# Kernel tuning notes

Hardware: AMD Instinct MI355X
Metric: run time of the kernel (lower is better)

Reference implementation:

```python
import jax, jax.numpy as jnp
import numpy as np

T = 8192
F = 128   # feature_size
H = 2048  # hidden_size
PRED_LEN = 12  # pred_length (fc_out head exists in module but is unused in forward)


def setup_inputs() -> dict:
    key = jax.random.key(0)
    ks = jax.random.split(key, 10)
    s_ih = 1.0 / np.sqrt(H)
    inp = {
        "x": jax.random.normal(ks[0], (T, F), dtype=jnp.float32),
        # PyTorch nn.LSTM params, gate order [i, f, g, o]
        "W_ih": jax.random.uniform(ks[1], (4 * H, F), jnp.float32, -s_ih, s_ih),
        "W_hh": jax.random.uniform(ks[2], (4 * H, H), jnp.float32, -s_ih, s_ih),
        "b_ih": jax.random.uniform(ks[3], (4 * H,), jnp.float32, -s_ih, s_ih),
        "b_hh": jax.random.uniform(ks[4], (4 * H,), jnp.float32, -s_ih, s_ih),
        # self.linear: Linear(H, H)
        "W_lin": jax.random.uniform(ks[5], (H, H), jnp.float32, -s_ih, s_ih),
        "b_lin": jax.random.uniform(ks[6], (H,), jnp.float32, -s_ih, s_ih),
        # self.one_out: Linear(H, 2)
        "W_out": jax.random.uniform(ks[7], (2, H), jnp.float32, -s_ih, s_ih),
        "b_out": jax.random.uniform(ks[8], (2,), jnp.float32, -s_ih, s_ih),
    }
    return inp


def _lstm_last_h(x, W_ih, W_hh, b_ih, b_hh):
    # x: [T, F]; returns final hidden state h: [H]
    # Precompute input projections for all timesteps: [T, 4H]
    x_proj = x @ W_ih.T + (b_ih + b_hh)

    def step(carry, xp):
        h, c = carry
        gates = xp + h @ W_hh.T  # [4H]
        i = jax.nn.sigmoid(gates[0 * H:1 * H])
        f = jax.nn.sigmoid(gates[1 * H:2 * H])
        g = jnp.tanh(gates[2 * H:3 * H])
        o = jax.nn.sigmoid(gates[3 * H:4 * H])
        c = f * c + i * g
        h = o * jnp.tanh(c)
        return (h, c), None

    h0 = jnp.zeros((H,), x.dtype)
    c0 = jnp.zeros((H,), x.dtype)
    (h, _), _ = jax.lax.scan(step, (h0, c0), x_proj)
    return h


def reference(x, W_ih, W_hh, b_ih, b_hh, W_lin, b_lin, W_out, b_out):
    h = _lstm_last_h(x, W_ih, W_hh, b_ih, b_hh)        # [H]
    y = h @ W_lin.T + b_lin                            # [H]
    y = y @ W_out.T + b_out                            # [2]
    return y.reshape(1, 1, 2)                          # matches torch (1,1,2)
```

## Files before the change

### kernel.cpp

```cpp
#include <hip/hip_runtime.h>


#define H      2048
#define TSTEPS 8192
#define FEAT   128
#define NBLK   256
#define NTHR   512
#define RESET_TH 0x10000000u

typedef float vf4 __attribute__((ext_vector_type(4)));
typedef float vf2 __attribute__((ext_vector_type(2)));

__device__ __forceinline__ float sigm(float xv) {
  return __builtin_amdgcn_rcpf(1.0f + __expf(-xv));
}
__device__ __forceinline__ float tanh_(float xv) {
  return 1.0f - 2.0f * __builtin_amdgcn_rcpf(__expf(2.0f * xv) + 1.0f);
}

union F2U { unsigned long long u; float2 f; };

#define DECLG(g) vf4 w##g##_0, w##g##_1, w##g##_2, w##g##_3, \
                     w##g##_4, w##g##_5, w##g##_6, w##g##_7; \
                 vf2 wih##g; float bias##g; float acc##g;

#define LOADG(g) { \
  const int row_ = (g) * H + j; \
  const float* wr_ = W_hh + (long)row_ * H; \
  w##g##_0 = *(const vf4*)(wr_ + 4*(ln      )); \
  w##g##_1 = *(const vf4*)(wr_ + 4*(ln +  64)); \
  w##g##_2 = *(const vf4*)(wr_ + 4*(ln + 128)); \
  w##g##_3 = *(const vf4*)(wr_ + 4*(ln + 192)); \
  w##g##_4 = *(const vf4*)(wr_ + 4*(ln + 256)); \
  w##g##_5 = *(const vf4*)(wr_ + 4*(ln + 320)); \
  w##g##_6 = *(const vf4*)(wr_ + 4*(ln + 384)); \
  w##g##_7 = *(const vf4*)(wr_ + 4*(ln + 448)); \
  wih##g  = *(const vf2*)(W_ih + (long)row_ * FEAT + 2*ln); \
  bias##g = b_ih[row_] + b_hh[row_]; }

#define PIN(g) asm volatile("" : \
  "+v"(w##g##_0), "+v"(w##g##_1), "+v"(w##g##_2), "+v"(w##g##_3), \
  "+v"(w##g##_4), "+v"(w##g##_5), "+v"(w##g##_6), "+v"(w##g##_7), \
  "+v"(wih##g), "+v"(bias##g));

#define STAGE_CHUNK(k, src, ldsrow) { \
  F2U lo_, hi_; \
  const float* p_ = (src) + 4*(ln + 64*(k)); \
  lo_.u = __hip_atomic_load((const unsigned long long*)p_, \
                            __ATOMIC_RELAXED, __HIP_MEMORY_SCOPE_AGENT); \
  hi_.u = __hip_atomic_load((const unsigned long long*)(p_ + 2), \
                            __ATOMIC_RELAXED, __HIP_MEMORY_SCOPE_AGENT); \
  vf4 t_; t_.x = lo_.f.x; t_.y = lo_.f.y; t_.z = hi_.f.x; t_.w = hi_.f.y; \
  *(vf4*)&(ldsrow)[4*(ln + 64*(k))] = t_; }

#define LDSREAD(k, ldsrow) \
  const vf4 hv##k = *(const vf4*)&(ldsrow)[4*(ln + 64*(k))];

#define FMA_G(g, c) \
  acc##g = __builtin_fmaf(w##g##_##c.x, h4_.x, acc##g); \
  acc##g = __builtin_fmaf(w##g##_##c.y, h4_.y, acc##g); \
  acc##g = __builtin_fmaf(w##g##_##c.z, h4_.z, acc##g); \
  acc##g = __builtin_fmaf(w##g##_##c.w, h4_.w, acc##g);

#define FMA_C(c) { const vf4 h4_ = hv##c; \
  FMA_G(0, c) FMA_G(1, c) FMA_G(2, c) FMA_G(3, c) }

#define REDUCE(g) { float a_ = acc##g; \
  a_ += __shfl_xor(a_, 1);  a_ += __shfl_xor(a_, 2);  a_ += __shfl_xor(a_, 4); \
  a_ += __shfl_xor(a_, 8);  a_ += __shfl_xor(a_, 16); a_ += __shfl_xor(a_, 32); \
  acc##g = a_ + bias##g; }

__global__ __launch_bounds__(NTHR, 2)
void lstm_persist(const float* __restrict__ x,
                  const float* __restrict__ W_ih,
                  const float* __restrict__ W_hh,
                  const float* __restrict__ b_ih,
                  const float* __restrict__ b_hh,
                  const float* __restrict__ W_lin,
                  const float* __restrict__ b_lin,
                  const float* __restrict__ W_out,
                  const float* __restrict__ b_out,
                  float* __restrict__ out,
                  float* __restrict__ ws)
{
  const int tid = threadIdx.x;
  const int b   = blockIdx.x;
  const int wv  = tid >> 6;
  const int ln  = tid & 63;

  float* hbuf0 = ws;
  float* hbuf1 = ws + H;
  float* ylin  = ws + 2 * H;
  unsigned* leaves = (unsigned*)(ws + 4 * H);
  unsigned* myleaf = leaves + (b & 7) * 64;

  __shared__ __align__(16) float h_lds[2][H];

  if (tid == 0 && b < 8) {
    if (__hip_atomic_load(leaves + b * 64, __ATOMIC_RELAXED,
                          __HIP_MEMORY_SCOPE_AGENT) >= RESET_TH)
      __hip_atomic_store(leaves + b * 64, 0u, __ATOMIC_RELAXED,
                         __HIP_MEMORY_SCOPE_AGENT);
  }
  if (tid < 8) {
    while (__hip_atomic_load(leaves + tid * 64, __ATOMIC_RELAXED,
                             __HIP_MEMORY_SCOPE_AGENT) >= RESET_TH) {
      __builtin_amdgcn_s_sleep(1);
    }
  }

  *(vf4*)&h_lds[0][4 * tid] = (vf4)(0.0f);

  const int j = b * 8 + wv;
  DECLG(0) DECLG(1) DECLG(2) DECLG(3)
  LOADG(0) LOADG(1) LOADG(2) LOADG(3)
  PIN(0) PIN(1) PIN(2) PIN(3)

  __syncthreads();

  float cst = 0.0f;

  #pragma unroll 1
  for (int t = 0; t < TSTEPS; ++t) {
    const vf2 xr = *(const vf2*)(x + (long)t * FEAT + 2 * ln);
    float* ldsrow = h_lds[t & 1];

    if (t > 0 && wv == 0) {
      const unsigned target = 32u * (unsigned)t;
      if (ln < 8) {
        const unsigned* lp = leaves + ln * 64;
        while (__hip_atomic_load(lp, __ATOMIC_RELAXED,
                                 __HIP_MEMORY_SCOPE_AGENT) < target) {
          __builtin_amdgcn_s_sleep(1);
        }
      }
      __builtin_amdgcn_fence(__ATOMIC_ACQUIRE, "workgroup");
      const float* hsrc = (t & 1) ? hbuf1 : hbuf0;
      STAGE_CHUNK(0, hsrc, ldsrow) STAGE_CHUNK(1, hsrc, ldsrow)
      STAGE_CHUNK(2, hsrc, ldsrow) STAGE_CHUNK(3, hsrc, ldsrow)
      STAGE_CHUNK(4, hsrc, ldsrow) STAGE_CHUNK(5, hsrc, ldsrow)
      STAGE_CHUNK(6, hsrc, ldsrow) STAGE_CHUNK(7, hsrc, ldsrow)
    }
    __syncthreads();

    LDSREAD(0, ldsrow) LDSREAD(1, ldsrow) LDSREAD(2, ldsrow) LDSREAD(3, ldsrow)
    LDSREAD(4, ldsrow) LDSREAD(5, ldsrow) LDSREAD(6, ldsrow) LDSREAD(7, ldsrow)

    acc0 = wih0.x * xr.x + wih0.y * xr.y;
    acc1 = wih1.x * xr.x + wih1.y * xr.y;
    acc2 = wih2.x * xr.x + wih2.y * xr.y;
    acc3 = wih3.x * xr.x + wih3.y * xr.y;

    FMA_C(0) FMA_C(1) FMA_C(2) FMA_C(3)
    FMA_C(4) FMA_C(5) FMA_C(6) FMA_C(7)

    REDUCE(0) REDUCE(1) REDUCE(2) REDUCE(3)

    const float iv = sigm(acc0);
    const float fv = sigm(acc1);
    const float gv = tanh_(acc2);
    const float ov = sigm(acc3);
    cst = fv * cst + iv * gv;
    const float hval = ov * tanh_(cst);

    if (ln == 0) {
      float* hdst = ((t + 1) & 1) ? hbuf1 : hbuf0;
      __hip_atomic_store(hdst + j, hval, __ATOMIC_RELAXED,
                         __HIP_MEMORY_SCOPE_AGENT);
    }
    __syncthreads();
    if (tid == 0) {
      __hip_atomic_fetch_add(myleaf, 1u, __ATOMIC_RELAXED,
                             __HIP_MEMORY_SCOPE_AGENT);
    }
  }

  {
    float* ldsrow = h_lds[0];
    if (wv == 0) {
      const unsigned target = 32u * (unsigned)TSTEPS;
      if (ln < 8) {
        const unsigned* lp = leaves + ln * 64;
        while (__hip_atomic_load(lp, __ATOMIC_RELAXED,
                                 __HIP_MEMORY_SCOPE_AGENT) < target) {
          __builtin_amdgcn_s_sleep(1);
        }
      }
      __builtin_amdgcn_fence(__ATOMIC_ACQUIRE, "workgroup");
      const float* hsrc = hbuf0;
      STAGE_CHUNK(0, hsrc, ldsrow) STAGE_CHUNK(1, hsrc, ldsrow)
      STAGE_CHUNK(2, hsrc, ldsrow) STAGE_CHUNK(3, hsrc, ldsrow)
      STAGE_CHUNK(4, hsrc, ldsrow) STAGE_CHUNK(5, hsrc, ldsrow)
      STAGE_CHUNK(6, hsrc, ldsrow) STAGE_CHUNK(7, hsrc, ldsrow)
    }
    __syncthreads();

    float a0 = 0.0f;
    const float* wl = W_lin + (long)j * H;
    #pragma unroll
    for (int k = 0; k < 8; ++k) {
      const vf4 h4 = *(const vf4*)&ldsrow[4 * (ln + 64 * k)];
      const vf4 u  = *(const vf4*)(wl + 4 * (ln + 64 * k));
      a0 += u.x * h4.x + u.y * h4.y + u.z * h4.z + u.w * h4.w;
    }
    a0 += __shfl_xor(a0, 1);  a0 += __shfl_xor(a0, 2);  a0 += __shfl_xor(a0, 4);
    a0 += __shfl_xor(a0, 8);  a0 += __shfl_xor(a0, 16); a0 += __shfl_xor(a0, 32);

    if (ln == 0) {
      __hip_atomic_store(ylin + j, a0 + b_lin[j], __ATOMIC_RELAXED,
                         __HIP_MEMORY_SCOPE_AGENT);
    }
    __syncthreads();
    if (tid == 0) {
      __hip_atomic_fetch_add(myleaf, 1u, __ATOMIC_RELAXED,
                             __HIP_MEMORY_SCOPE_AGENT);
    }
  }

  if (b == 0 && wv == 0) {
    const unsigned target = 32u * (unsigned)(TSTEPS + 1);
    if (ln < 8) {
      const unsigned* lp = leaves + ln * 64;
      while (__hip_atomic_load(lp, __ATOMIC_RELAXED,
                               __HIP_MEMORY_SCOPE_AGENT) < target) {
        __builtin_amdgcn_s_sleep(1);
      }
    }
    __builtin_amdgcn_fence(__ATOMIC_ACQUIRE, "workgroup");
    float p0 = 0.0f, p1 = 0.0f;
    #pragma unroll
    for (int k = 0; k < 8; ++k) {
      const int c = 4 * (ln + 64 * k);
      F2U ylo, yhi;
      ylo.u = __hip_atomic_load((const unsigned long long*)(ylin + c),
                                __ATOMIC_RELAXED, __HIP_MEMORY_SCOPE_AGENT);
      yhi.u = __hip_atomic_load((const unsigned long long*)(ylin + c + 2),
                                __ATOMIC_RELAXED, __HIP_MEMORY_SCOPE_AGENT);
      const float4 yv = make_float4(ylo.f.x, ylo.f.y, yhi.f.x, yhi.f.y);
      const vf4 q0 = *(const vf4*)(W_out + c);
      const vf4 q1 = *(const vf4*)(W_out + H + c);
      p0 += q0.x * yv.x + q0.y * yv.y + q0.z * yv.z + q0.w * yv.w;
      p1 += q1.x * yv.x + q1.y * yv.y + q1.z * yv.z + q1.w * yv.w;
    }
    p0 += __shfl_xor(p0, 1);  p0 += __shfl_xor(p0, 2);  p0 += __shfl_xor(p0, 4);
    p0 += __shfl_xor(p0, 8);  p0 += __shfl_xor(p0, 16); p0 += __shfl_xor(p0, 32);
    p1 += __shfl_xor(p1, 1);  p1 += __shfl_xor(p1, 2);  p1 += __shfl_xor(p1, 4);
    p1 += __shfl_xor(p1, 8);  p1 += __shfl_xor(p1, 16); p1 += __shfl_xor(p1, 32);
    if (ln == 0) {
      out[0] = p0 + b_out[0];
      out[1] = p1 + b_out[1];
    }
  }
}

extern "C" void kernel_launch(void* const* d_in, const int* in_sizes, int n_in,
                              void* d_out, int out_size, void* d_ws, size_t ws_size,
                              hipStream_t stream) {
  const float* x     = (const float*)d_in[0];
  const float* W_ih  = (const float*)d_in[1];
  const float* W_hh  = (const float*)d_in[2];
  const float* b_ih  = (const float*)d_in[3];
  const float* b_hh  = (const float*)d_in[4];
  const float* W_lin = (const float*)d_in[5];
  const float* b_lin = (const float*)d_in[6];
  const float* W_out = (const float*)d_in[7];
  const float* b_out = (const float*)d_in[8];

  lstm_persist<<<dim3(NBLK), dim3(NTHR), 0, stream>>>(
      x, W_ih, W_hh, b_ih, b_hh, W_lin, b_lin, W_out, b_out,
      (float*)d_out, (float*)d_ws);
}
```

Measured before the change: 37.45 ms.

## Replace counter barrier with step tags packed alongside hidden values

Each hidden value is now written as a 64-bit word holding the float and its timestep tag. Consumers poll the data words themselves until every tag matches, instead of waiting on eight leaf counters that are bumped with atomics. This removes the per-step trailing __syncthreads, the fetch_add, and the counter-reset prologue, which shortens the critical path between LSTM steps. In exchange, every block polls 2048 64-bit words per step rather than eight counters, so polling traffic to L2 rises. Correctness across repeated launches now relies on stale tags never matching the expected step.

```diff
diff --git a/kernel.cpp b/kernel.cpp
--- a/kernel.cpp
+++ b/kernel.cpp
@@ -6,10 +6,10 @@
 #define FEAT   128
 #define NBLK   256
 #define NTHR   512
-#define RESET_TH 0x10000000u
 
 typedef float vf4 __attribute__((ext_vector_type(4)));
 typedef float vf2 __attribute__((ext_vector_type(2)));
+typedef unsigned long long u64;
 
 __device__ __forceinline__ float sigm(float xv) {
   return __builtin_amdgcn_rcpf(1.0f + __expf(-xv));
@@ -17,8 +17,6 @@
 __device__ __forceinline__ float tanh_(float xv) {
   return 1.0f - 2.0f * __builtin_amdgcn_rcpf(__expf(2.0f * xv) + 1.0f);
 }
-
-union F2U { unsigned long long u; float2 f; };
 
 #define DECLG(g) vf4 w##g##_0, w##g##_1, w##g##_2, w##g##_3, \
                      w##g##_4, w##g##_5, w##g##_6, w##g##_7; \
@@ -43,16 +41,6 @@
   "+v"(w##g##_4), "+v"(w##g##_5), "+v"(w##g##_6), "+v"(w##g##_7), \
   "+v"(wih##g), "+v"(bias##g));
 
-#define STAGE_CHUNK(k, src, ldsrow) { \
-  F2U lo_, hi_; \
-  const float* p_ = (src) + 4*(ln + 64*(k)); \
-  lo_.u = __hip_atomic_load((const unsigned long long*)p_, \
-                            __ATOMIC_RELAXED, __HIP_MEMORY_SCOPE_AGENT); \
-  hi_.u = __hip_atomic_load((const unsigned long long*)(p_ + 2), \
-                            __ATOMIC_RELAXED, __HIP_MEMORY_SCOPE_AGENT); \
-  vf4 t_; t_.x = lo_.f.x; t_.y = lo_.f.y; t_.z = hi_.f.x; t_.w = hi_.f.y; \
-  *(vf4*)&(ldsrow)[4*(ln + 64*(k))] = t_; }
-
 #define LDSREAD(k, ldsrow) \
   const vf4 hv##k = *(const vf4*)&(ldsrow)[4*(ln + 64*(k))];
 
@@ -69,6 +57,33 @@
   a_ += __shfl_xor(a_, 1);  a_ += __shfl_xor(a_, 2);  a_ += __shfl_xor(a_, 4); \
   a_ += __shfl_xor(a_, 8);  a_ += __shfl_xor(a_, 16); a_ += __shfl_xor(a_, 32); \
   acc##g = a_ + bias##g; }
+
+__device__ __forceinline__ void stage_poll(const u64* __restrict__ buf,
+                                           unsigned tg,
+                                           float* __restrict__ ldsrow,
+                                           int ln) {
+  u64 pv[32];
+  #pragma unroll
+  for (int k = 0; k < 32; ++k)
+    pv[k] = __hip_atomic_load(buf + ln + 64 * k, __ATOMIC_RELAXED,
+                              __HIP_MEMORY_SCOPE_AGENT);
+  while (true) {
+    int ok = 1;
+    #pragma unroll
+    for (int k = 0; k < 32; ++k)
+      ok &= ((unsigned)pv[k] == tg) ? 1 : 0;
+    if (__all(ok)) break;
+    __builtin_amdgcn_s_sleep(1);
+    #pragma unroll
+    for (int k = 0; k < 32; ++k)
+      if ((unsigned)pv[k] != tg)
+        pv[k] = __hip_atomic_load(buf + ln + 64 * k, __ATOMIC_RELAXED,
+                                  __HIP_MEMORY_SCOPE_AGENT);
+  }
+  #pragma unroll
+  for (int k = 0; k < 32; ++k)
+    ldsrow[ln + 64 * k] = __uint_as_float((unsigned)(pv[k] >> 32));
+}
 
 __global__ __launch_bounds__(NTHR, 2)
 void lstm_persist(const float* __restrict__ x,
@@ -88,26 +103,10 @@
   const int wv  = tid >> 6;
   const int ln  = tid & 63;
 
-  float* hbuf0 = ws;
-  float* hbuf1 = ws + H;
-  float* ylin  = ws + 2 * H;
-  unsigned* leaves = (unsigned*)(ws + 4 * H);
-  unsigned* myleaf = leaves + (b & 7) * 64;
+  u64* buf0 = (u64*)ws;
+  u64* buf1 = buf0 + H;
 
   __shared__ __align__(16) float h_lds[2][H];
-
-  if (tid == 0 && b < 8) {
-    if (__hip_atomic_load(leaves + b * 64, __ATOMIC_RELAXED,
-                          __HIP_MEMORY_SCOPE_AGENT) >= RESET_TH)
-      __hip_atomic_store(leaves + b * 64, 0u, __ATOMIC_RELAXED,
-                         __HIP_MEMORY_SCOPE_AGENT);
-  }
-  if (tid < 8) {
-    while (__hip_atomic_load(leaves + tid * 64, __ATOMIC_RELAXED,
-                             __HIP_MEMORY_SCOPE_AGENT) >= RESET_TH) {
-      __builtin_amdgcn_s_sleep(1);
-    }
-  }
 
   *(vf4*)&h_lds[0][4 * tid] = (vf4)(0.0f);
 
@@ -125,22 +124,8 @@
     const vf2 xr = *(const vf2*)(x + (long)t * FEAT + 2 * ln);
     float* ldsrow = h_lds[t & 1];
 
-    if (t > 0 && wv == 0) {
-      const unsigned target = 32u * (unsigned)t;
-      if (ln < 8) {
-        const unsigned* lp = leaves + ln * 64;
-        while (__hip_atomic_load(lp, __ATOMIC_RELAXED,
-                                 __HIP_MEMORY_SCOPE_AGENT) < target) {
-          __builtin_amdgcn_s_sleep(1);
-        }
-      }
-      __builtin_amdgcn_fence(__ATOMIC_ACQUIRE, "workgroup");
-      const float* hsrc = (t & 1) ? hbuf1 : hbuf0;
-      STAGE_CHUNK(0, hsrc, ldsrow) STAGE_CHUNK(1, hsrc, ldsrow)
-      STAGE_CHUNK(2, hsrc, ldsrow) STAGE_CHUNK(3, hsrc, ldsrow)
-      STAGE_CHUNK(4, hsrc, ldsrow) STAGE_CHUNK(5, hsrc, ldsrow)
-      STAGE_CHUNK(6, hsrc, ldsrow) STAGE_CHUNK(7, hsrc, ldsrow)
-    }
+    if (t > 0 && wv == 0)
+      stage_poll((t & 1) ? buf1 : buf0, (unsigned)t, ldsrow, ln);
     __syncthreads();
 
     LDSREAD(0, ldsrow) LDSREAD(1, ldsrow) LDSREAD(2, ldsrow) LDSREAD(3, ldsrow)
@@ -164,35 +149,18 @@
     const float hval = ov * tanh_(cst);
 
     if (ln == 0) {
-      float* hdst = ((t + 1) & 1) ? hbuf1 : hbuf0;
-      __hip_atomic_store(hdst + j, hval, __ATOMIC_RELAXED,
+      u64* dst = (((t + 1) & 1) ? buf1 : buf0) + j;
+      const u64 pack = ((u64)__float_as_uint(hval) << 32)
+                     | (unsigned)(t + 1);
+      __hip_atomic_store(dst, pack, __ATOMIC_RELAXED,
                          __HIP_MEMORY_SCOPE_AGENT);
-    }
-    __syncthreads();
-    if (tid == 0) {
-      __hip_atomic_fetch_add(myleaf, 1u, __ATOMIC_RELAXED,
-                             __HIP_MEMORY_SCOPE_AGENT);
     }
   }
 
   {
     float* ldsrow = h_lds[0];
-    if (wv == 0) {
-      const unsigned target = 32u * (unsigned)TSTEPS;
-      if (ln < 8) {
-        const unsigned* lp = leaves + ln * 64;
-        while (__hip_atomic_load(lp, __ATOMIC_RELAXED,
-                                 __HIP_MEMORY_SCOPE_AGENT) < target) {
-          __builtin_amdgcn_s_sleep(1);
-        }
-      }
-      __builtin_amdgcn_fence(__ATOMIC_ACQUIRE, "workgroup");
-      const float* hsrc = hbuf0;
-      STAGE_CHUNK(0, hsrc, ldsrow) STAGE_CHUNK(1, hsrc, ldsrow)
-      STAGE_CHUNK(2, hsrc, ldsrow) STAGE_CHUNK(3, hsrc, ldsrow)
-      STAGE_CHUNK(4, hsrc, ldsrow) STAGE_CHUNK(5, hsrc, ldsrow)
-      STAGE_CHUNK(6, hsrc, ldsrow) STAGE_CHUNK(7, hsrc, ldsrow)
-    }
+    if (wv == 0)
+      stage_poll(buf0, (unsigned)TSTEPS, ldsrow, ln);
     __syncthreads();
 
     float a0 = 0.0f;
@@ -207,40 +175,40 @@
     a0 += __shfl_xor(a0, 8);  a0 += __shfl_xor(a0, 16); a0 += __shfl_xor(a0, 32);
 
     if (ln == 0) {
-      __hip_atomic_store(ylin + j, a0 + b_lin[j], __ATOMIC_RELAXED,
+      const float yv = a0 + b_lin[j];
+      const u64 pack = ((u64)__float_as_uint(yv) << 32)
+                     | (unsigned)(TSTEPS + 1);
+      __hip_atomic_store(buf1 + j, pack, __ATOMIC_RELAXED,
                          __HIP_MEMORY_SCOPE_AGENT);
     }
-    __syncthreads();
-    if (tid == 0) {
-      __hip_atomic_fetch_add(myleaf, 1u, __ATOMIC_RELAXED,
-                             __HIP_MEMORY_SCOPE_AGENT);
-    }
   }
 
   if (b == 0 && wv == 0) {
-    const unsigned target = 32u * (unsigned)(TSTEPS + 1);
-    if (ln < 8) {
-      const unsigned* lp = leaves + ln * 64;
-      while (__hip_atomic_load(lp, __ATOMIC_RELAXED,
-                               __HIP_MEMORY_SCOPE_AGENT) < target) {
-        __builtin_amdgcn_s_sleep(1);
-      }
-    }
-    __builtin_amdgcn_fence(__ATOMIC_ACQUIRE, "workgroup");
+    u64 pv[32];
+    #pragma unroll
+    for (int k = 0; k < 32; ++k)
+      pv[k] = __hip_atomic_load(buf1 + ln + 64 * k, __ATOMIC_RELAXED,
+                                __HIP_MEMORY_SCOPE_AGENT);
+    while (true) {
+      int ok = 1;
+      #pragma unroll
+      for (int k = 0; k < 32; ++k)
+        ok &= ((unsigned)pv[k] == (unsigned)(TSTEPS + 1)) ? 1 : 0;
+      if (__all(ok)) break;
+      __builtin_amdgcn_s_sleep(1);
+      #pragma unroll
+      for (int k = 0; k < 32; ++k)
+        if ((unsigned)pv[k] != (unsigned)(TSTEPS + 1))
+          pv[k] = __hip_atomic_load(buf1 + ln + 64 * k, __ATOMIC_RELAXED,
+                                    __HIP_MEMORY_SCOPE_AGENT);
+    }
     float p0 = 0.0f, p1 = 0.0f;
     #pragma unroll
-    for (int k = 0; k < 8; ++k) {
-      const int c = 4 * (ln + 64 * k);
-      F2U ylo, yhi;
-      ylo.u = __hip_atomic_load((const unsigned long long*)(ylin + c),
-                                __ATOMIC_RELAXED, __HIP_MEMORY_SCOPE_AGENT);
-      yhi.u = __hip_atomic_load((const unsigned long long*)(ylin + c + 2),
-                                __ATOMIC_RELAXED, __HIP_MEMORY_SCOPE_AGENT);
-      const float4 yv = make_float4(ylo.f.x, ylo.f.y, yhi.f.x, yhi.f.y);
-      const vf4 q0 = *(const vf4*)(W_out + c);
-      const vf4 q1 = *(const vf4*)(W_out + H + c);
-      p0 += q0.x * yv.x + q0.y * yv.y + q0.z * yv.z + q0.w * yv.w;
-      p1 += q1.x * yv.x + q1.y * yv.y + q1.z * yv.z + q1.w * yv.w;
+    for (int k = 0; k < 32; ++k) {
+      const int c = ln + 64 * k;
+      const float yv = __uint_as_float((unsigned)(pv[k] >> 32));
+      p0 = __builtin_fmaf(W_out[c],     yv, p0);
+      p1 = __builtin_fmaf(W_out[H + c], yv, p1);
     }
     p0 += __shfl_xor(p0, 1);  p0 += __shfl_xor(p0, 2);  p0 += __shfl_xor(p0, 4);
     p0 += __shfl_xor(p0, 8);  p0 += __shfl_xor(p0, 16); p0 += __shfl_xor(p0, 32);
```

New measurement: 66.22 ms. 76.8% more time.
